# Kernel optimization log

Hardware: AMD Instinct MI355X
Metric: run time of the kernel (lower is better)

Reference implementation:

```python
import jax, jax.numpy as jnp
import numpy as np
from jax import lax

B, T, D, U = 128, 1024, 256, 48


def setup_inputs() -> dict:
    key = jax.random.key(0)
    k1, k2, k3 = jax.random.split(key, 3)
    x = jax.random.normal(k1, (B, T, D), dtype=jnp.float32)
    kernel = jax.random.normal(k2, (D, U), dtype=jnp.float32) * (1.0 / np.sqrt(D))
    bias = jnp.zeros((U,), dtype=jnp.float32)
    chain_kernel = jax.random.normal(k3, (U, U), dtype=jnp.float32)
    return {"x": x, "kernel": kernel, "bias": bias, "chain_kernel": chain_kernel}


def _viterbi_decode(logits, trans):
    # logits: [B, T, U], trans: [U, U]; full-length sequences (mask=None)
    init_state = logits[:, 0]  # [B, U]
    steps = jnp.swapaxes(logits[:, 1:], 0, 1)  # [T-1, B, U]

    def fwd(state, logit_t):
        # scores[b, i, j] = state[b, i] + trans[i, j]
        scores = state[:, :, None] + trans[None]  # [B, U, U]
        bp = jnp.argmax(scores, axis=1)            # [B, U] best prev tag
        new_state = logit_t + jnp.max(scores, axis=1)
        return new_state, bp

    final_state, bps = lax.scan(fwd, init_state, steps)  # bps: [T-1, B, U]
    last_tag = jnp.argmax(final_state, axis=-1)          # [B]

    def back(tag, bp):
        prev = jnp.take_along_axis(bp, tag[:, None], axis=1)[:, 0]
        return prev, prev

    # reverse scan emits tags for t = 0..T-2 in forward time order
    _, tags_head = lax.scan(back, last_tag, bps, reverse=True)  # [T-1, B]
    tags = jnp.concatenate([tags_head, last_tag[None]], axis=0)  # [T, B]
    return jnp.transpose(tags)  # [B, T]


def reference(x, kernel, bias, chain_kernel):
    # _dense_layer: linear activation -> x @ kernel + bias
    logits = jnp.einsum('btd,du->btu', x, kernel) + bias  # [B, T, U]
    pred_ids = _viterbi_decode(logits, chain_kernel)       # [B, T] int
    return pred_ids.astype(jnp.float32)
```

## Files before the change

### kernel.cpp

```cpp
#include <hip/hip_runtime.h>
#include <cstdint>

#define B_ 128
#define T_ 1024
#define D_ 256
#define U_ 48

typedef float v2f __attribute__((ext_vector_type(2)));

__device__ __forceinline__ v2f pk_add(v2f a, v2f b) {
    v2f d;
    asm("v_pk_add_f32 %0, %1, %2" : "=v"(d) : "v"(a), "v"(b));
    return d;
}
__device__ __forceinline__ float max3f(float a, float b, float c) {
    float d;
    asm("v_max3_f32 %0, %1, %2, %3" : "=v"(d) : "v"(a), "v"(b), "v"(c));
    return d;
}

__global__ __launch_bounds__(256, 1) void k_logits(const float* __restrict__ x,
                                                   const float* __restrict__ kern,
                                                   const float* __restrict__ bias,
                                                   float* __restrict__ logits) {
    __shared__ float K[D_ * U_];
    __shared__ float bsh[U_];
    const int tid = threadIdx.x;
    for (int i = tid; i < D_ * U_; i += 256) K[i] = kern[i];
    if (tid < U_) bsh[tid] = bias[tid];
    __syncthreads();

    const long row0 = (long)blockIdx.x * 256 + tid;
    const long row1 = row0 + (long)B_ * T_ / 2;
    const float4* xr0 = (const float4*)(x + row0 * D_);
    const float4* xr1 = (const float4*)(x + row1 * D_);

    float a0[U_], a1[U_];
#pragma unroll
    for (int u = 0; u < U_; ++u) { a0[u] = 0.0f; a1[u] = 0.0f; }

#pragma unroll 1
    for (int blk = 0; blk < D_ / 32; ++blk) {
        float4 xa[8], xb[8];
#pragma unroll
        for (int i = 0; i < 8; ++i) xa[i] = xr0[blk * 8 + i];
#pragma unroll
        for (int i = 0; i < 8; ++i) xb[i] = xr1[blk * 8 + i];

#pragma unroll
        for (int i = 0; i < 8; ++i) {
            const int d4 = blk * 8 + i;
            const float xc0[4] = {xa[i].x, xa[i].y, xa[i].z, xa[i].w};
            const float xc1[4] = {xb[i].x, xb[i].y, xb[i].z, xb[i].w};
#pragma unroll
            for (int c = 0; c < 4; ++c) {
                const float4* kp = (const float4*)&K[(d4 * 4 + c) * U_];
                const float s0 = xc0[c], s1 = xc1[c];
#pragma unroll
                for (int u4 = 0; u4 < U_ / 4; ++u4) {
                    float4 kv = kp[u4];
                    a0[u4*4+0] += s0 * kv.x;  a1[u4*4+0] += s1 * kv.x;
                    a0[u4*4+1] += s0 * kv.y;  a1[u4*4+1] += s1 * kv.y;
                    a0[u4*4+2] += s0 * kv.z;  a1[u4*4+2] += s1 * kv.z;
                    a0[u4*4+3] += s0 * kv.w;  a1[u4*4+3] += s1 * kv.w;
                }
            }
        }
    }

    float4* o0 = (float4*)(logits + row0 * U_);
    float4* o1 = (float4*)(logits + row1 * U_);
#pragma unroll
    for (int i = 0; i < U_ / 4; ++i) {
        float4 v0, v1;
        v0.x = a0[i*4+0] + bsh[i*4+0];  v1.x = a1[i*4+0] + bsh[i*4+0];
        v0.y = a0[i*4+1] + bsh[i*4+1];  v1.y = a1[i*4+1] + bsh[i*4+1];
        v0.z = a0[i*4+2] + bsh[i*4+2];  v1.z = a1[i*4+2] + bsh[i*4+2];
        v0.w = a0[i*4+3] + bsh[i*4+3];  v1.w = a1[i*4+3] + bsh[i*4+3];
        o0[i] = v0;
        o1[i] = v1;
    }
}

__device__ __forceinline__ float step_max_lds(const float4* sb, const v2f* tc2) {
    float4 s[12];
#pragma unroll
    for (int k = 0; k < 12; ++k) s[k] = sb[k];
    float cf[48];
#pragma unroll
    for (int k = 0; k < 12; ++k) {
        v2f lo, hi;
        lo.x = s[k].x; lo.y = s[k].y;
        hi.x = s[k].z; hi.y = s[k].w;
        v2f r0 = pk_add(lo, tc2[2 * k + 0]);
        v2f r1 = pk_add(hi, tc2[2 * k + 1]);
        cf[4*k+0] = r0.x; cf[4*k+1] = r0.y;
        cf[4*k+2] = r1.x; cf[4*k+3] = r1.y;
    }
    float t1[16];
#pragma unroll
    for (int i = 0; i < 16; ++i) t1[i] = max3f(cf[3*i], cf[3*i+1], cf[3*i+2]);
    float t2[6];
#pragma unroll
    for (int i = 0; i < 5; ++i) t2[i] = max3f(t1[3*i], t1[3*i+1], t1[3*i+2]);
    t2[5] = t1[15];
    const float a = max3f(t2[0], t2[1], t2[2]);
    const float b = max3f(t2[3], t2[4], t2[5]);
    return fmaxf(a, b);
}

__global__ __launch_bounds__(64, 1) void k_forward(const float* __restrict__ trans,
                                                   const float* __restrict__ logits,
                                                   float* __restrict__ delta) {
    __shared__ float4 sbuf[2][U_ / 4];
    const int lane = threadIdx.x;
    const int b = blockIdx.x;
    const int u = (lane < U_) ? lane : (U_ - 1);

    v2f tc2[U_ / 2];
#pragma unroll
    for (int v = 0; v < U_; v += 2) {
        tc2[v / 2].x = trans[v * U_ + u];
        tc2[v / 2].y = trans[(v + 1) * U_ + u];
    }

    const float* lin = logits + (long)b * T_ * U_;
    float* dout = delta + (long)b * T_ * U_;

    float state = lin[u];
    dout[u] = state;
    ((float*)sbuf[0])[u] = state;

    float pf[8];
#pragma unroll
    for (int i = 0; i < 8; ++i) pf[i] = lin[(1 + i) * U_ + u];

    const float* lp = lin + 9 * U_ + u;
    float* dp = dout + 1 * U_ + u;

#pragma unroll 1
    for (int g = 0; g < 127; ++g) {
#pragma unroll
        for (int j = 0; j < 8; ++j) {
            const float logit = pf[j];
            pf[j] = lp[j * U_];

            const float4* sb = sbuf[j & 1];
            const float m = step_max_lds(sb, tc2);
            state = logit + m;
            ((float*)sbuf[(j & 1) ^ 1])[u] = state;
            dp[j * U_] = state;
        }
        lp += 8 * U_;
        dp += 8 * U_;
    }

#pragma unroll
    for (int j = 0; j < 7; ++j) {
        const float logit = pf[j];
        const float4* sb = sbuf[j & 1];
        const float m = step_max_lds(sb, tc2);
        state = logit + m;
        ((float*)sbuf[(j & 1) ^ 1])[u] = state;
        dp[j * U_] = state;
    }
}

__global__ __launch_bounds__(64, 1) void k_forward_inplace(const float* __restrict__ trans,
                                                           float* __restrict__ delta) {
    __shared__ float4 sbuf[2][U_ / 4];
    const int lane = threadIdx.x;
    const int b = blockIdx.x;
    const int u = (lane < U_) ? lane : (U_ - 1);

    v2f tc2[U_ / 2];
#pragma unroll
    for (int v = 0; v < U_; v += 2) {
        tc2[v / 2].x = trans[v * U_ + u];
        tc2[v / 2].y = trans[(v + 1) * U_ + u];
    }

    float* base = delta + (long)b * T_ * U_;
    float state = base[u];
    ((float*)sbuf[0])[u] = state;

#pragma unroll 1
    for (int t = 1; t < T_; ++t) {
        const float logit = base[(long)t * U_ + u];
        const float m = step_max_lds(sbuf[(t - 1) & 1], tc2);
        state = logit + m;
        ((float*)sbuf[t & 1])[u] = state;
        base[(long)t * U_ + u] = state;
    }
}

#define BP_ROWS 32
__global__ __launch_bounds__(64, 1) void k_bp(const float* __restrict__ trans,
                                              const float* __restrict__ delta,
                                              unsigned char* __restrict__ bp) {
    __shared__ float sbuf[2][U_];
    const int lane = threadIdx.x;
    const int u = (lane < U_) ? lane : (U_ - 1);

    float tc[U_];
#pragma unroll
    for (int v = 0; v < U_; ++v) tc[v] = trans[v * U_ + u];

    const int NROW = B_ * (T_ - 1);
    const int row0 = blockIdx.x * BP_ROWS;
    if (row0 >= NROW) return;

    int b = row0 / (T_ - 1);
    int tm1 = row0 - b * (T_ - 1);

    float dval = delta[((long)b * T_ + tm1) * U_ + u];

#pragma unroll 1
    for (int i = 0; i < BP_ROWS; ++i) {
        const int row = row0 + i;
        if (row >= NROW) break;

        sbuf[i & 1][u] = dval;

        int bn = b, tn = tm1 + 1;
        if (tn == T_ - 1) { tn = 0; bn = b + 1; }
        float dnext = 0.0f;
        if (row + 1 < NROW) dnext = delta[((long)bn * T_ + tn) * U_ + u];

        const float4* sb4 = (const float4*)sbuf[i & 1];
        float best = -3.4e38f;
        int bi = 0;
#pragma unroll
        for (int k = 0; k < U_ / 4; ++k) {
            float4 s = sb4[k];
            float c0 = s.x + tc[4*k+0];
            float c1 = s.y + tc[4*k+1];
            float c2 = s.z + tc[4*k+2];
            float c3 = s.w + tc[4*k+3];
            bi = (c0 > best) ? 4*k+0 : bi;  best = fmaxf(best, c0);
            bi = (c1 > best) ? 4*k+1 : bi;  best = fmaxf(best, c1);
            bi = (c2 > best) ? 4*k+2 : bi;  best = fmaxf(best, c2);
            bi = (c3 > best) ? 4*k+3 : bi;  best = fmaxf(best, c3);
        }
        bp[(long)row * U_ + u] = (unsigned char)bi;

        b = bn; tm1 = tn; dval = dnext;
    }
}

__global__ __launch_bounds__(64) void k_back(const float* __restrict__ delta,
                                             const unsigned char* __restrict__ bp,
                                             float* __restrict__ out) {
    __shared__ unsigned char bpl[(T_ - 1) * U_];
    __shared__ float tags[T_];
    __shared__ float fin[U_];
    const int lane = threadIdx.x;
    const int b = blockIdx.x;

    const uint32_t* src = (const uint32_t*)(bp + (long)b * (T_ - 1) * U_);
    uint32_t* dst = (uint32_t*)bpl;
    const int NW = (T_ - 1) * U_ / 4;
    for (int i = lane; i < NW; i += 64) dst[i] = src[i];
    if (lane < U_) fin[lane] = delta[((long)b * T_ + (T_ - 1)) * U_ + lane];
    __syncthreads();

    if (lane == 0) {
        float best = fin[0];
        int tag = 0;
        for (int uu = 1; uu < U_; ++uu)
            if (fin[uu] > best) { best = fin[uu]; tag = uu; }
        tags[T_ - 1] = (float)tag;
        for (int t = T_ - 1; t >= 1; --t) {
            tag = bpl[(t - 1) * U_ + tag];
            tags[t - 1] = (float)tag;
        }
    }
    __syncthreads();

    float* o = out + (long)b * T_;
    for (int i = lane; i < T_; i += 64) o[i] = tags[i];
}

extern "C" void kernel_launch(void* const* d_in, const int* in_sizes, int n_in,
                              void* d_out, int out_size, void* d_ws, size_t ws_size,
                              hipStream_t stream) {
    const float* x     = (const float*)d_in[0];
    const float* kern  = (const float*)d_in[1];
    const float* bias  = (const float*)d_in[2];
    const float* trans = (const float*)d_in[3];
    float* out = (float*)d_out;

    const size_t NBT = (size_t)B_ * T_ * U_ * sizeof(float);

    float* logits = (float*)d_ws;
    const bool two_buf = ws_size >= 2 * NBT + (size_t)B_ * T_ * U_;
    float* delta = two_buf ? (float*)((char*)d_ws + NBT) : logits;
    unsigned char* bp = (unsigned char*)d_ws + (two_buf ? 2 * NBT : NBT);

    const int NROW = B_ * (T_ - 1);
    const int bp_grid = (NROW + BP_ROWS - 1) / BP_ROWS;

    k_logits<<<(B_ * T_ / 2) / 256, 256, 0, stream>>>(x, kern, bias, logits);
    if (two_buf)
        k_forward<<<B_, 64, 0, stream>>>(trans, logits, delta);
    else
        k_forward_inplace<<<B_, 64, 0, stream>>>(trans, logits);
    k_bp  <<<bp_grid, 64, 0, stream>>>(trans, delta, bp);
    k_back<<<B_,      64, 0, stream>>>(delta, bp, out);
}
```

Before: 529.4 us.

## Parallelize Viterbi backtrace with blockwise pointer-jumping composition

Replaces the single-thread serial backtrace over 1023 steps with a three-phase scheme. First, all threads compose the backpointer maps over 32 blocks of 32 steps for every possible end tag. Then one thread chains the 32 block maps, and 32 threads expand each block in parallel. This shortens the serial dependency chain of dependent LDS loads, at the cost of more total lookups and a 256-thread block. A padded identity row handles the last block, and the argmax now uses a wave shuffle.

After: 500.4 us. -5.5%, faster.

```diff
diff --git a/kernel.cpp b/kernel.cpp
--- a/kernel.cpp
+++ b/kernel.cpp
@@ -248,37 +248,84 @@
     }
 }
 
-__global__ __launch_bounds__(64) void k_back(const float* __restrict__ delta,
-                                             const unsigned char* __restrict__ bp,
-                                             float* __restrict__ out) {
-    __shared__ unsigned char bpl[(T_ - 1) * U_];
+#define KB_ 32
+#define NB_ 32
+__global__ __launch_bounds__(256) void k_back(const float* __restrict__ delta,
+                                              const unsigned char* __restrict__ bp,
+                                              float* __restrict__ out) {
+    __shared__ unsigned char bpl[1024 * U_];
+    __shared__ unsigned char gmap[NB_ * U_];
+    __shared__ unsigned char eIn[NB_];
     __shared__ float tags[T_];
-    __shared__ float fin[U_];
-    const int lane = threadIdx.x;
+    __shared__ int Ash;
+    const int tid = threadIdx.x;
     const int b = blockIdx.x;
 
     const uint32_t* src = (const uint32_t*)(bp + (long)b * (T_ - 1) * U_);
     uint32_t* dst = (uint32_t*)bpl;
     const int NW = (T_ - 1) * U_ / 4;
-    for (int i = lane; i < NW; i += 64) dst[i] = src[i];
-    if (lane < U_) fin[lane] = delta[((long)b * T_ + (T_ - 1)) * U_ + lane];
-    __syncthreads();
-
-    if (lane == 0) {
-        float best = fin[0];
-        int tag = 0;
-        for (int uu = 1; uu < U_; ++uu)
-            if (fin[uu] > best) { best = fin[uu]; tag = uu; }
-        tags[T_ - 1] = (float)tag;
-        for (int t = T_ - 1; t >= 1; --t) {
-            tag = bpl[(t - 1) * U_ + tag];
-            tags[t - 1] = (float)tag;
+    for (int i = tid; i < NW; i += 256) dst[i] = src[i];
+    if (tid < U_) bpl[1023 * U_ + tid] = (unsigned char)tid;
+
+    if (tid < 64) {
+        const int lane = tid;
+        float v = (lane < U_) ? delta[((long)b * T_ + (T_ - 1)) * U_ + lane] : -3.4e38f;
+        int idx = (lane < U_) ? lane : 64;
+#pragma unroll
+        for (int off = 32; off >= 1; off >>= 1) {
+            const float ov = __shfl_xor(v, off);
+            const int oi = __shfl_xor(idx, off);
+            if (ov > v || (ov == v && oi < idx)) { v = ov; idx = oi; }
+        }
+        if (lane == 0) Ash = idx;
+    }
+    __syncthreads();
+
+    int ik[6], ek[6], ck[6];
+#pragma unroll
+    for (int k = 0; k < 6; ++k) {
+        const int tau = tid + k * 256;
+        ik[k] = tau / U_;
+        ek[k] = tau - ik[k] * U_;
+        ck[k] = ek[k];
+    }
+#pragma unroll
+    for (int h = 0; h < KB_; ++h) {
+#pragma unroll
+        for (int k = 0; k < 6; ++k) {
+            const int r = ik[k] * KB_ + (KB_ - 1 - h);
+            ck[k] = bpl[r * U_ + ck[k]];
+        }
+    }
+#pragma unroll
+    for (int k = 0; k < 6; ++k) gmap[ik[k] * U_ + ek[k]] = (unsigned char)ck[k];
+    __syncthreads();
+
+    if (tid == 0) {
+        int cur = Ash;
+        eIn[NB_ - 1] = (unsigned char)cur;
+#pragma unroll 1
+        for (int i = NB_ - 1; i >= 1; --i) {
+            cur = gmap[i * U_ + cur];
+            eIn[i - 1] = (unsigned char)cur;
+        }
+    }
+    __syncthreads();
+
+    if (tid < NB_) {
+        const int i = tid;
+        int cur = eIn[i];
+#pragma unroll
+        for (int h = 0; h < KB_; ++h) {
+            const int r = i * KB_ + (KB_ - 1 - h);
+            cur = bpl[r * U_ + cur];
+            tags[r] = (float)cur;
         }
     }
     __syncthreads();
 
     float* o = out + (long)b * T_;
-    for (int i = lane; i < T_; i += 64) o[i] = tags[i];
+    for (int i = tid; i < T_; i += 256) o[i] = tags[i];
 }
 
 extern "C" void kernel_launch(void* const* d_in, const int* in_sizes, int n_in,
@@ -306,5 +353,5 @@
     else
         k_forward_inplace<<<B_, 64, 0, stream>>>(trans, logits);
     k_bp  <<<bp_grid, 64, 0, stream>>>(trans, delta, bp);
-    k_back<<<B_,      64, 0, stream>>>(delta, bp, out);
-}
+    k_back<<<B_, 256, 0, stream>>>(delta, bp, out);
+}
```
